# Kernel optimization log

Measured on AMD Instinct MI355X. Metric: run time of the kernel, lower is better.

The kernel has to match this reference:

```python
import jax, jax.numpy as jnp
import numpy as np


def setup_inputs() -> dict:
    key = jax.random.key(0)
    B, T, N = 16, 1024, 4096
    input_current = jax.random.normal(key, (B, T, N), dtype=jnp.float32)
    tau_mem = jnp.ones((1,), dtype=jnp.float32) * 20.0
    return {"input_current": input_current, "tau_mem": tau_mem}


def reference(input_current, tau_mem):
    # ExpLeak: state_t = alpha * state_{t-1} + x_t, alpha = exp(-1/tau_mem)
    # initial state is zeros of shape (B, *feature_dims)
    alpha = jnp.exp(-1.0 / tau_mem)[0]  # scalar
    x_t_first = jnp.swapaxes(input_current, 0, 1)  # [T, B, N]
    init_state = jnp.zeros(x_t_first.shape[1:], dtype=input_current.dtype)

    def step(state, x):
        new_state = alpha * state + x
        return new_state, new_state

    _, out = jax.lax.scan(step, init_state, x_t_first)  # [T, B, N]
    return jnp.swapaxes(out, 0, 1)  # [B, T, N]
```

## Files before the change

kernel.cpp:

```cpp
#include <hip/hip_runtime.h>


constexpr int T = 1024;
constexpr int N = 4096;
constexpr int B = 16;
constexpr int N4 = N / 4;
constexpr int TS = 32;
constexpr int SEC = T / TS;

__device__ __forceinline__ float4 fma4(float a, float4 s, float4 x) {
  float4 r;
  r.x = fmaf(a, s.x, x.x);
  r.y = fmaf(a, s.y, x.y);
  r.z = fmaf(a, s.z, x.z);
  r.w = fmaf(a, s.w, x.w);
  return r;
}

__global__ __launch_bounds__(1024) void k_partial(
    const float4* __restrict__ in4, const float* __restrict__ tau_mem,
    float4* __restrict__ out4) {
  const int b = blockIdx.x / SEC;
  const int s = blockIdx.x % SEC;
  const int n4 = threadIdx.x;
  const float alpha = expf(-1.0f / tau_mem[0]);
  const size_t base = (size_t)(b * T + s * TS) * N4 + n4;
  float4 S = make_float4(0.f, 0.f, 0.f, 0.f);
#pragma unroll 8
  for (int j = 0; j < TS; ++j) {
    S = fma4(alpha, S, in4[base + (size_t)j * N4]);
  }
  out4[base] = S;
}

__global__ __launch_bounds__(256) void k_scan(
    float4* __restrict__ out4, const float* __restrict__ tau_mem) {
  const int t = blockIdx.x * blockDim.x + threadIdx.x;
  if (t >= B * N4) return;
  const int b = t >> 10;
  const int n4 = t & (N4 - 1);
  const float aTS = expf(-(float)TS / tau_mem[0]);
  float4* col = out4 + (size_t)b * T * N4 + n4;
  float4 C = make_float4(0.f, 0.f, 0.f, 0.f);
  for (int s = 0; s < SEC; ++s) {
    const size_t off = (size_t)(s * TS) * N4;
    float4 e = col[off];
    col[off] = C;
    C = fma4(aTS, C, e);
  }
}

__global__ __launch_bounds__(1024) void k_apply(
    const float4* __restrict__ in4, const float* __restrict__ tau_mem,
    float4* __restrict__ out4) {
  const int b = blockIdx.x / SEC;
  const int s = blockIdx.x % SEC;
  const int n4 = threadIdx.x;
  const float alpha = expf(-1.0f / tau_mem[0]);
  const size_t base = (size_t)(b * T + s * TS) * N4 + n4;
  float4 S = out4[base];
#pragma unroll 4
  for (int j = 0; j < TS; ++j) {
    S = fma4(alpha, S, in4[base + (size_t)j * N4]);
    out4[base + (size_t)j * N4] = S;
  }
}

extern "C" void kernel_launch(void* const* d_in, const int* in_sizes, int n_in,
                              void* d_out, int out_size, void* d_ws, size_t ws_size,
                              hipStream_t stream) {
  const float4* in4 = (const float4*)d_in[0];
  const float* tau = (const float*)d_in[1];
  float4* out4 = (float4*)d_out;

  k_partial<<<B * SEC, 1024, 0, stream>>>(in4, tau, out4);
  k_scan<<<(B * N4) / 256, 256, 0, stream>>>(out4, tau);
  k_apply<<<B * SEC, 1024, 0, stream>>>(in4, tau, out4);
}
```

Baseline: 495.7 us.

## Use workspace for chunk partials, fold carry scan into apply, nontemporal stores

When a large enough workspace is supplied, chunk partial sums go to a compact buffer instead of the output. The separate carry-scan kernel is dropped: each apply block recomputes its incoming carry by serially combining the preceding chunk partials. Output stores become nontemporal so they do not push the re-read input out of cache. This removes one kernel launch and the scattered in-place scan traffic, but later chunks redo up to 31 extra partial reads each, and the fallback path only runs when no workspace is available.

```diff
diff --git a/kernel.cpp b/kernel.cpp
--- a/kernel.cpp
+++ b/kernel.cpp
@@ -8,6 +8,8 @@
 constexpr int TS = 32;
 constexpr int SEC = T / TS;
 
+typedef float floatx4 __attribute__((ext_vector_type(4)));
+
 __device__ __forceinline__ float4 fma4(float a, float4 s, float4 x) {
   float4 r;
   r.x = fmaf(a, s.x, x.x);
@@ -17,7 +19,55 @@
   return r;
 }
 
-__global__ __launch_bounds__(1024) void k_partial(
+__device__ __forceinline__ void nt_store4(float4 v, float4* p) {
+  floatx4 t;
+  t.x = v.x; t.y = v.y; t.z = v.z; t.w = v.w;
+  __builtin_nontemporal_store(t, reinterpret_cast<floatx4*>(p));
+}
+
+
+__global__ __launch_bounds__(1024) void k_partial_ws(
+    const float4* __restrict__ in4, const float* __restrict__ tau_mem,
+    float4* __restrict__ part4) {
+  const int b = blockIdx.x / SEC;
+  const int s = blockIdx.x % SEC;
+  const int n4 = threadIdx.x;
+  const float alpha = expf(-1.0f / tau_mem[0]);
+  const size_t base = (size_t)(b * T + s * TS) * N4 + n4;
+  float4 S = make_float4(0.f, 0.f, 0.f, 0.f);
+#pragma unroll 8
+  for (int j = 0; j < TS; ++j) {
+    S = fma4(alpha, S, in4[base + (size_t)j * N4]);
+  }
+  part4[(size_t)(b * SEC + s) * N4 + n4] = S;
+}
+
+__global__ __launch_bounds__(1024) void k_apply_ws(
+    const float4* __restrict__ in4, const float* __restrict__ tau_mem,
+    const float4* __restrict__ part4, float4* __restrict__ out4) {
+  const int b = blockIdx.x / SEC;
+  const int s = blockIdx.x % SEC;
+  const int n4 = threadIdx.x;
+  const float alpha = expf(-1.0f / tau_mem[0]);
+  const float aTS = expf(-(float)TS / tau_mem[0]);
+
+  float4 C = make_float4(0.f, 0.f, 0.f, 0.f);
+  const float4* ebase = part4 + (size_t)(b * SEC) * N4 + n4;
+  for (int j = 0; j < s; ++j) {
+    C = fma4(aTS, C, ebase[(size_t)j * N4]);
+  }
+
+  const size_t base = (size_t)(b * T + s * TS) * N4 + n4;
+  float4 S = C;
+#pragma unroll 4
+  for (int j = 0; j < TS; ++j) {
+    S = fma4(alpha, S, in4[base + (size_t)j * N4]);
+    nt_store4(S, &out4[base + (size_t)j * N4]);
+  }
+}
+
+
+__global__ __launch_bounds__(1024) void k_partial_ip(
     const float4* __restrict__ in4, const float* __restrict__ tau_mem,
     float4* __restrict__ out4) {
   const int b = blockIdx.x / SEC;
@@ -33,7 +83,7 @@
   out4[base] = S;
 }
 
-__global__ __launch_bounds__(256) void k_scan(
+__global__ __launch_bounds__(256) void k_scan_ip(
     float4* __restrict__ out4, const float* __restrict__ tau_mem) {
   const int t = blockIdx.x * blockDim.x + threadIdx.x;
   if (t >= B * N4) return;
@@ -50,7 +100,7 @@
   }
 }
 
-__global__ __launch_bounds__(1024) void k_apply(
+__global__ __launch_bounds__(1024) void k_apply_ip(
     const float4* __restrict__ in4, const float* __restrict__ tau_mem,
     float4* __restrict__ out4) {
   const int b = blockIdx.x / SEC;
@@ -73,7 +123,14 @@
   const float* tau = (const float*)d_in[1];
   float4* out4 = (float4*)d_out;
 
-  k_partial<<<B * SEC, 1024, 0, stream>>>(in4, tau, out4);
-  k_scan<<<(B * N4) / 256, 256, 0, stream>>>(out4, tau);
-  k_apply<<<B * SEC, 1024, 0, stream>>>(in4, tau, out4);
+  const size_t need = (size_t)B * SEC * N * sizeof(float);
+  if (d_ws != nullptr && ws_size >= need) {
+    float4* part4 = (float4*)d_ws;
+    k_partial_ws<<<B * SEC, 1024, 0, stream>>>(in4, tau, part4);
+    k_apply_ws<<<B * SEC, 1024, 0, stream>>>(in4, tau, part4, out4);
+  } else {
+    k_partial_ip<<<B * SEC, 1024, 0, stream>>>(in4, tau, out4);
+    k_scan_ip<<<(B * N4) / 256, 256, 0, stream>>>(out4, tau);
+    k_apply_ip<<<B * SEC, 1024, 0, stream>>>(in4, tau, out4);
+  }
 }
```

Result: no change. 496.7 us (+0.2%).
